# Performance work log

Measured on AMD Instinct MI355X. Metric: run time of the kernel, lower is better.

Reference implementation:

```python
import jax, jax.numpy as jnp
import numpy as np

N = 50000   # nodes
E = 100000  # directed edges
G = 2048    # graphs in batch
D = 32      # hidden dim
F_NODE = 11
F_EDGE = 4


def setup_inputs() -> dict:
    key = jax.random.key(0)
    ks = jax.random.split(key, 12)
    s = 0.1
    return {
        "x": jax.random.normal(ks[0], (N, F_NODE), dtype=jnp.float32),
        "edge_attr": jax.random.uniform(ks[1], (E, F_EDGE), dtype=jnp.float32),
        "lin0_w": jax.random.normal(ks[2], (D, F_NODE), dtype=jnp.float32) * s,
        "lin0_b": jnp.zeros((D,), jnp.float32),
        "nn_w": jax.random.normal(ks[3], (D * D, F_EDGE), dtype=jnp.float32) * s,
        "nn_b": jnp.zeros((D * D,), jnp.float32),
        "root_w": jax.random.normal(ks[4], (D, D), dtype=jnp.float32) * s,
        "conv_b": jnp.zeros((D,), jnp.float32),
        "gru_wi": jax.random.normal(ks[5], (3 * D, D), dtype=jnp.float32) * s,
        "gru_wh": jax.random.normal(ks[6], (3 * D, D), dtype=jnp.float32) * s,
        "gru_bi": jnp.zeros((3 * D,), jnp.float32),
        "gru_bh": jnp.zeros((3 * D,), jnp.float32),
        "lin1_w": jax.random.normal(ks[7], (2, D), dtype=jnp.float32) * s,
        "lin1_b": jnp.zeros((2,), jnp.float32),
        "edge_index": jax.random.randint(ks[8], (2, E), 0, N, dtype=jnp.int32),
        "batch": jnp.sort(jax.random.randint(ks[9], (N,), 0, G, dtype=jnp.int32)),
    }


def _gru_step(m, h, wi, wh, bi, bh):
    # single-step torch.nn.GRU cell math
    gi = m @ wi.T + bi            # [N, 3D]
    gh = h @ wh.T + bh            # [N, 3D]
    ir, iz, inn = jnp.split(gi, 3, axis=-1)
    hr, hz, hn = jnp.split(gh, 3, axis=-1)
    r = jax.nn.sigmoid(ir + hr)
    z = jax.nn.sigmoid(iz + hz)
    n = jnp.tanh(inn + r * hn)
    return (1.0 - z) * n + z * h


def reference(x, edge_attr, lin0_w, lin0_b, nn_w, nn_b, root_w, conv_b,
              gru_wi, gru_wh, gru_bi, gru_bh, lin1_w, lin1_b,
              edge_index, batch):
    src, dst = edge_index[0], edge_index[1]
    out = jax.nn.relu(x @ lin0_w.T + lin0_b)   # [N, D]
    h = out
    # per-edge 32x32 weight from edge MLP (edge_attr fixed -> hoisted out of loop)
    W_e = (edge_attr @ nn_w.T + nn_b).reshape(E, D, D)
    for _ in range(3):
        msg = jnp.einsum('ei,eio->eo', out[src], W_e)                  # [E, D]
        aggr = jax.ops.segment_sum(msg, dst, num_segments=N)           # add-aggregate
        m = jax.nn.relu(aggr + out @ root_w + conv_b)                  # NNConv root + bias
        h = _gru_step(m, h, gru_wi, gru_wh, gru_bi, gru_bh)
        out = h
    cnt = jax.ops.segment_sum(jnp.ones((N,), x.dtype), batch, num_segments=G)
    pooled = jax.ops.segment_sum(out, batch, num_segments=G) / jnp.maximum(cnt, 1.0)[:, None]
    logits = pooled @ lin1_w.T + lin1_b                                # [G, 2]
    return jax.nn.log_softmax(logits, axis=1)
```

## Files before the change

### kernel.cpp

```cpp
#include <hip/hip_runtime.h>
#include <hip/hip_bf16.h>

#define NN 50000
#define EE 100000
#define GG 2048
#define NB2 391

typedef float v2f __attribute__((ext_vector_type(2)));
__device__ __forceinline__ v2f fma2(v2f a, float b, v2f c) {
    return __builtin_elementwise_fma(a, (v2f){b, b}, c);
}

__device__ __forceinline__ float b2f(unsigned short u) {
    union { unsigned int i; float f; } x; x.i = (unsigned int)u << 16; return x.f;
}
__device__ __forceinline__ unsigned short f2b(float f) {
    union { float f; unsigned int i; } x; x.f = f;
    unsigned int b = x.i + (0x7FFFu + ((x.i >> 16) & 1u));
    return (unsigned short)(b >> 16);
}

__global__ __launch_bounds__(256) void k_setup(
    const float* __restrict__ x, const float* __restrict__ lw,
    const float* __restrict__ lb, const float* __restrict__ nnw,
    const float* __restrict__ nnb, const float* __restrict__ rootw,
    const float* __restrict__ wi, const float* __restrict__ wh,
    const int* __restrict__ ei, float* __restrict__ feat,
    float* __restrict__ Wre, float4* __restrict__ rw4,
    float4* __restrict__ wi4, int* __restrict__ cnt) {
    int blk = blockIdx.x;
    int t = threadIdx.x;
    if (blk < 6250) {
        int idx = blk * 256 + t;
        if (idx >= NN * 32) return;
        int n = idx >> 5, o = idx & 31;
        const float* xr = x + n * 11;
        const float* wr = lw + o * 11;
        float acc = lb[o];
#pragma unroll
        for (int i = 0; i < 11; ++i) acc += xr[i] * wr[i];
        feat[idx] = fmaxf(acc, 0.f);
    } else if (blk < 6278) {
        int idx = (blk - 6250) * 256 + t;
        if (idx < 5120) {
            int c = idx >> 5, i = idx & 31;
            float v;
            if (c < 128) v = nnw[((i << 5) + (c & 31)) * 4 + (c >> 5)];
            else         v = nnb[(i << 5) + (c - 128)];
            Wre[idx] = v;
        } else if (idx < 6144) {
            int j = idx - 5120;
            int k = j >> 5, o = j & 31;
            rw4[j] = make_float4(rootw[k * 32 + o], wh[o * 32 + k],
                                 wh[(32 + o) * 32 + k], wh[(64 + o) * 32 + k]);
        } else if (idx < 7168) {
            int j = idx - 6144;
            int k = j >> 5, o = j & 31;
            wi4[j] = make_float4(wi[o * 32 + k], wi[(32 + o) * 32 + k],
                                 wi[(64 + o) * 32 + k], 0.f);
        }
    } else {
        int e = (blk - 6278) * 256 + t;
        if (e >= EE) return;
        atomicAdd(&cnt[ei[EE + e]], 1);
        atomicAdd(&cnt[NN + ei[e]], 1);
    }
}

__global__ __launch_bounds__(256) void k_scan1(const int* __restrict__ cnt,
                                               int* __restrict__ tmp,
                                               int* __restrict__ bsum) {
    __shared__ int sd[256];
    int t = threadIdx.x;
    int i = blockIdx.x * 256 + t;
    int v = (i < 2 * NN) ? cnt[i] : 0;
    sd[t] = v;
    __syncthreads();
#pragma unroll
    for (int off = 1; off < 256; off <<= 1) {
        int x = (t >= off) ? sd[t - off] : 0;
        __syncthreads();
        sd[t] += x;
        __syncthreads();
    }
    if (i < 2 * NN) tmp[i] = sd[t];
    if (t == 255) bsum[blockIdx.x] = sd[255];
}

__global__ __launch_bounds__(512) void k_scan2(int* __restrict__ bsum) {
    __shared__ int sd[512];
    int t = threadIdx.x;
    int v = (t < NB2) ? bsum[t] : 0;
    sd[t] = v;
    __syncthreads();
#pragma unroll
    for (int off = 1; off < 512; off <<= 1) {
        int x = (t >= off) ? sd[t - off] : 0;
        __syncthreads();
        sd[t] += x;
        __syncthreads();
    }
    if (t < NB2) bsum[t] = sd[t];
}

__global__ void k_scan3(const int* __restrict__ cnt, const int* __restrict__ tmp,
                        const int* __restrict__ bsum, int* __restrict__ row_ptr,
                        int* __restrict__ cursor, int* __restrict__ out_ptr,
                        int* __restrict__ cursor2) {
    int i = blockIdx.x * blockDim.x + threadIdx.x;
    if (i >= 2 * NN) return;
    int base = (blockIdx.x > 0) ? bsum[blockIdx.x - 1] : 0;
    int excl = base + tmp[i] - cnt[i];
    if (i < NN) {
        row_ptr[i] = excl;
        cursor[i] = excl;
        if (i == 0) row_ptr[NN] = EE;
    } else {
        int j = i - NN;
        out_ptr[j] = excl - EE;
        cursor2[j] = excl - EE;
        if (j == 0) out_ptr[NN] = EE;
    }
}

__global__ __launch_bounds__(256) void k_scatter_y(
    const int* __restrict__ ei, const float* __restrict__ ea,
    int* __restrict__ cursor, int* __restrict__ cursor2,
    int* __restrict__ esrc, float4* __restrict__ eea,
    int* __restrict__ oslot, float4* __restrict__ oea,
    const float* __restrict__ feat, const float* __restrict__ Wre,
    unsigned short* __restrict__ yb) {
    int blk = blockIdx.x;
    if (blk < 391) {
        int e = blk * 256 + threadIdx.x;
        if (e >= EE) return;
        int s = ei[e], d = ei[EE + e];
        float4 a = make_float4(ea[e * 4 + 0], ea[e * 4 + 1], ea[e * 4 + 2], ea[e * 4 + 3]);
        int slot = atomicAdd(&cursor[d], 1);
        esrc[slot] = s;
        eea[slot] = a;
        int pos = atomicAdd(&cursor2[s], 1);
        oslot[pos] = slot;
        oea[pos] = a;
        return;
    }
    int by = blk - 391;
    int bx = by % 782, q = by / 782;
    int lane = threadIdx.x & 63;
    int wv = __builtin_amdgcn_readfirstlane(threadIdx.x >> 6);
    int n = bx * 64 + lane;
    if (n >= NN) return;
    int c0 = q * 40 + wv * 10;
    float fr[32];
    const float4* f4 = (const float4*)(feat + (long)n * 32);
#pragma unroll
    for (int qq = 0; qq < 8; ++qq) {
        float4 v = f4[qq];
        fr[4 * qq + 0] = v.x; fr[4 * qq + 1] = v.y;
        fr[4 * qq + 2] = v.z; fr[4 * qq + 3] = v.w;
    }
    float acc[10];
#pragma unroll
    for (int cc = 0; cc < 10; ++cc) {
        const float* w = Wre + (c0 + cc) * 32;
        float a = 0.f;
#pragma unroll
        for (int i = 0; i < 32; ++i) a += fr[i] * w[i];
        acc[cc] = a;
    }
    unsigned short* yr = yb + (long)n * 160 + c0;
#pragma unroll
    for (int qq = 0; qq < 5; ++qq) {
        unsigned int wlo = f2b(acc[2 * qq]);
        unsigned int whi = f2b(acc[2 * qq + 1]);
        ((unsigned int*)yr)[qq] = wlo | (whi << 16);
    }
}

__global__ __launch_bounds__(256) void k_conv_update(
    const unsigned short* __restrict__ msg_in, const int* __restrict__ row_ptr,
    const float4* __restrict__ rw4, const float* __restrict__ convb,
    const float4* __restrict__ wi4, const float* __restrict__ bi,
    const float* __restrict__ bh, const float4* __restrict__ nnw4,
    const float* __restrict__ nnb, const int* __restrict__ out_ptr,
    const int* __restrict__ oslot, const float4* __restrict__ oea,
    const unsigned short* __restrict__ yb, const int* __restrict__ esrc,
    const float4* __restrict__ eea,
    float* __restrict__ feat, unsigned short* __restrict__ msg_out,
    int gather_from_y, int write_msg) {
    __shared__ float fsT[32][36];
    __shared__ float msT[32][36];
    int t = threadIdx.x;
    int g = t >> 5, o = t & 31;
    int gc = g * 4;
    int nb = blockIdx.x * 32 + gc;
    float f[4], m[4];
    float cb = convb[o];
#pragma unroll
    for (int j = 0; j < 4; ++j) {
        int n = nb + j;
        bool v = (n < NN);
        f[j] = v ? feat[n * 32 + o] : 0.f;
        m[j] = cb;
        if (v) {
            int e0 = row_ptr[n], e1 = row_ptr[n + 1];
            if (gather_from_y) {
                for (int e = e0; e < e1; ++e) {
                    int s = esrc[e];
                    float4 a = eea[e];
                    const unsigned short* yr = yb + (long)s * 160;
                    float y0 = b2f(yr[o]);
                    float y1 = b2f(yr[32 + o]);
                    float y2 = b2f(yr[64 + o]);
                    float y3 = b2f(yr[96 + o]);
                    float y4 = b2f(yr[128 + o]);
                    m[j] += y4 + a.x * y0 + a.y * y1 + a.z * y2 + a.w * y3;
                }
            } else {
                for (int e = e0; e < e1; ++e)
                    m[j] += b2f(msg_in[(e << 5) + o]);
            }
        }
    }
    *(float4*)&fsT[o][gc] = make_float4(f[0], f[1], f[2], f[3]);
    __syncthreads();

    float bhr = bh[o], bhz = bh[32 + o], bhn = bh[64 + o];
    v2f m01 = {m[0], m[1]}, m23 = {m[2], m[3]};
    v2f ghr01 = {bhr, bhr}, ghr23 = {bhr, bhr};
    v2f ghz01 = {bhz, bhz}, ghz23 = {bhz, bhz};
    v2f ghn01 = {bhn, bhn}, ghn23 = {bhn, bhn};
#pragma unroll 4
    for (int i = 0; i < 32; ++i) {
        float4 w = rw4[i * 32 + o];
        float4 fv = *(const float4*)&fsT[i][gc];
        v2f f01 = {fv.x, fv.y}, f23 = {fv.z, fv.w};
        m01 = fma2(f01, w.x, m01);   m23 = fma2(f23, w.x, m23);
        ghr01 = fma2(f01, w.y, ghr01); ghr23 = fma2(f23, w.y, ghr23);
        ghz01 = fma2(f01, w.z, ghz01); ghz23 = fma2(f23, w.z, ghz23);
        ghn01 = fma2(f01, w.w, ghn01); ghn23 = fma2(f23, w.w, ghn23);
    }
    float mm0 = fmaxf(m01.x, 0.f), mm1 = fmaxf(m01.y, 0.f);
    float mm2 = fmaxf(m23.x, 0.f), mm3 = fmaxf(m23.y, 0.f);
    *(float4*)&msT[o][gc] = make_float4(mm0, mm1, mm2, mm3);
    __syncthreads();

    float bir = bi[o], biz = bi[32 + o], bin_ = bi[64 + o];
    v2f gir01 = {bir, bir}, gir23 = {bir, bir};
    v2f giz01 = {biz, biz}, giz23 = {biz, biz};
    v2f gin01 = {bin_, bin_}, gin23 = {bin_, bin_};
#pragma unroll 4
    for (int k = 0; k < 32; ++k) {
        float4 w = wi4[k * 32 + o];
        float4 mv = *(const float4*)&msT[k][gc];
        v2f p01 = {mv.x, mv.y}, p23 = {mv.z, mv.w};
        gir01 = fma2(p01, w.x, gir01); gir23 = fma2(p23, w.x, gir23);
        giz01 = fma2(p01, w.y, giz01); giz23 = fma2(p23, w.y, giz23);
        gin01 = fma2(p01, w.z, gin01); gin23 = fma2(p23, w.z, gin23);
    }
    float girA[4] = {gir01.x, gir01.y, gir23.x, gir23.y};
    float gizA[4] = {giz01.x, giz01.y, giz23.x, giz23.y};
    float ginA[4] = {gin01.x, gin01.y, gin23.x, gin23.y};
    float ghrA[4] = {ghr01.x, ghr01.y, ghr23.x, ghr23.y};
    float ghzA[4] = {ghz01.x, ghz01.y, ghz23.x, ghz23.y};
    float ghnA[4] = {ghn01.x, ghn01.y, ghn23.x, ghn23.y};
    float fn[4];
#pragma unroll
    for (int j = 0; j < 4; ++j) {
        int n = nb + j;
        float r = 1.f / (1.f + __expf(-(girA[j] + ghrA[j])));
        float z = 1.f / (1.f + __expf(-(gizA[j] + ghzA[j])));
        float nt = tanhf(ginA[j] + r * ghnA[j]);
        fn[j] = (1.f - z) * nt + z * f[j];
        if (n < NN) feat[n * 32 + o] = fn[j];
    }
    if (!write_msg) return;

    *(float4*)&fsT[o][gc] = make_float4(fn[0], fn[1], fn[2], fn[3]);
    v2f y0_01 = {0.f, 0.f}, y0_23 = {0.f, 0.f};
    v2f y1_01 = {0.f, 0.f}, y1_23 = {0.f, 0.f};
    v2f y2_01 = {0.f, 0.f}, y2_23 = {0.f, 0.f};
    v2f y3_01 = {0.f, 0.f}, y3_23 = {0.f, 0.f};
    v2f y4_01 = {0.f, 0.f}, y4_23 = {0.f, 0.f};
#pragma unroll 4
    for (int i = 0; i < 32; ++i) {
        float4 w = nnw4[i * 32 + o];
        float w1 = nnb[i * 32 + o];
        float4 fv = *(const float4*)&fsT[i][gc];
        v2f f01 = {fv.x, fv.y}, f23 = {fv.z, fv.w};
        y0_01 = fma2(f01, w.x, y0_01); y0_23 = fma2(f23, w.x, y0_23);
        y1_01 = fma2(f01, w.y, y1_01); y1_23 = fma2(f23, w.y, y1_23);
        y2_01 = fma2(f01, w.z, y2_01); y2_23 = fma2(f23, w.z, y2_23);
        y3_01 = fma2(f01, w.w, y3_01); y3_23 = fma2(f23, w.w, y3_23);
        y4_01 = fma2(f01, w1, y4_01);  y4_23 = fma2(f23, w1, y4_23);
    }
    float ya0[4] = {y0_01.x, y0_01.y, y0_23.x, y0_23.y};
    float ya1[4] = {y1_01.x, y1_01.y, y1_23.x, y1_23.y};
    float ya2[4] = {y2_01.x, y2_01.y, y2_23.x, y2_23.y};
    float ya3[4] = {y3_01.x, y3_01.y, y3_23.x, y3_23.y};
    float ya4[4] = {y4_01.x, y4_01.y, y4_23.x, y4_23.y};
#pragma unroll
    for (int j = 0; j < 4; ++j) {
        int n = nb + j;
        if (n < NN) {
            int p0 = out_ptr[n], p1 = out_ptr[n + 1];
            for (int p = p0; p < p1; ++p) {
                float4 a = oea[p];
                int slot = oslot[p];
                msg_out[(slot << 5) + o] =
                    f2b(ya4[j] + a.x * ya0[j] + a.y * ya1[j]
                               + a.z * ya2[j] + a.w * ya3[j]);
            }
        }
    }
}

__global__ __launch_bounds__(64) void k_pool_final(
    const float* __restrict__ feat, const int* __restrict__ batch,
    const float* __restrict__ w, const float* __restrict__ b,
    float* __restrict__ out) {
    int g = blockIdx.x;
    int t = threadIdx.x;
    int o = t & 31, h = t >> 5;
    int lo = 0, hi = NN;
    while (lo < hi) { int mid = (lo + hi) >> 1; if (batch[mid] < g) lo = mid + 1; else hi = mid; }
    int start = lo;
    hi = NN;
    while (lo < hi) { int mid = (lo + hi) >> 1; if (batch[mid] <= g) lo = mid + 1; else hi = mid; }
    int end = lo;
    float acc = 0.f;
    for (int n = start + h; n < end; n += 2) acc += feat[(long)n * 32 + o];
    acc += __shfl_xor(acc, 32, 64);
    float p = acc / fmaxf((float)(end - start), 1.f);
    float l0 = p * w[o], l1 = p * w[32 + o];
#pragma unroll
    for (int s = 16; s >= 1; s >>= 1) {
        l0 += __shfl_xor(l0, s, 64);
        l1 += __shfl_xor(l1, s, 64);
    }
    if (t == 0) {
        l0 += b[0]; l1 += b[1];
        float mx = fmaxf(l0, l1);
        float lse = mx + logf(__expf(l0 - mx) + __expf(l1 - mx));
        out[g * 2 + 0] = l0 - lse;
        out[g * 2 + 1] = l1 - lse;
    }
}

extern "C" void kernel_launch(void* const* d_in, const int* in_sizes, int n_in,
                              void* d_out, int out_size, void* d_ws, size_t ws_size,
                              hipStream_t stream) {
    const float* x        = (const float*)d_in[0];
    const float* edge_attr= (const float*)d_in[1];
    const float* lin0_w   = (const float*)d_in[2];
    const float* lin0_b   = (const float*)d_in[3];
    const float* nn_w     = (const float*)d_in[4];
    const float* nn_b     = (const float*)d_in[5];
    const float* root_w   = (const float*)d_in[6];
    const float* conv_b   = (const float*)d_in[7];
    const float* gru_wi   = (const float*)d_in[8];
    const float* gru_wh   = (const float*)d_in[9];
    const float* gru_bi   = (const float*)d_in[10];
    const float* gru_bh   = (const float*)d_in[11];
    const float* lin1_w   = (const float*)d_in[12];
    const float* lin1_b   = (const float*)d_in[13];
    const int*   edge_idx = (const int*)d_in[14];
    const int*   batch    = (const int*)d_in[15];
    float* out = (float*)d_out;

    float4* rw4   = (float4*)d_ws;
    float4* wi4   = rw4 + 1024;
    float4* eea   = wi4 + 1024;
    float4* oea   = eea + EE;
    float*  feat  = (float*)(oea + EE);
    float*  Wre   = feat + (long)NN * 32;
    int*    cnt   = (int*)(Wre + 5120);
    int*    tmp   = cnt + 2 * NN;
    int*    bsum  = tmp + 2 * NN;
    int*    row_ptr = bsum + 512;
    int*    cursor  = row_ptr + NN + 1;
    int*    out_ptr = cursor + NN;
    int*    cursor2 = out_ptr + NN + 1;
    int*    esrc  = cursor2 + NN;
    int*    oslot = esrc + EE;
    unsigned short* yb   = (unsigned short*)(oslot + EE);
    unsigned short* msgA = yb + (long)NN * 160;
    unsigned short* msgB = msgA + (long)EE * 32;
    const float4* nnw4 = (const float4*)nn_w;

    hipMemsetAsync(cnt, 0, 2 * NN * sizeof(int), stream);

    k_setup<<<6250 + 28 + 391, 256, 0, stream>>>(x, lin0_w, lin0_b, nn_w, nn_b,
                                                 root_w, gru_wi, gru_wh, edge_idx,
                                                 feat, Wre, rw4, wi4, cnt);

    k_scan1<<<NB2, 256, 0, stream>>>(cnt, tmp, bsum);
    k_scan2<<<1, 512, 0, stream>>>(bsum);
    k_scan3<<<NB2, 256, 0, stream>>>(cnt, tmp, bsum, row_ptr, cursor, out_ptr, cursor2);

    k_scatter_y<<<391 + 782 * 4, 256, 0, stream>>>(edge_idx, edge_attr, cursor, cursor2,
                                                   esrc, eea, oslot, oea, feat, Wre, yb);

    k_conv_update<<<(NN + 31) / 32, 256, 0, stream>>>(msgA, row_ptr, rw4, conv_b, wi4,
                                                      gru_bi, gru_bh, nnw4, nn_b,
                                                      out_ptr, oslot, oea,
                                                      yb, esrc, eea,
                                                      feat, msgB, 1, 1);
    k_conv_update<<<(NN + 31) / 32, 256, 0, stream>>>(msgB, row_ptr, rw4, conv_b, wi4,
                                                      gru_bi, gru_bh, nnw4, nn_b,
                                                      out_ptr, oslot, oea,
                                                      yb, esrc, eea,
                                                      feat, msgA, 0, 1);
    k_conv_update<<<(NN + 31) / 32, 256, 0, stream>>>(msgA, row_ptr, rw4, conv_b, wi4,
                                                      gru_bi, gru_bh, nnw4, nn_b,
                                                      out_ptr, oslot, oea,
                                                      yb, esrc, eea,
                                                      feat, msgB, 0, 0);

    k_pool_final<<<GG, 64, 0, stream>>>(feat, batch, lin1_w, lin1_b, out);
}
```

Measured before the change: 266.4 us.

## Template conv-update on nodes per group and store edge messages in fp32

The conv/GRU update kernel is now templated on nodes per thread group. Layers 2 and 3 use 8 nodes per group (64 per block) so each weight load is reused across more nodes, while layer 1 keeps 4. The per-edge message buffers switch from bf16 to fp32, which removes the pack and unpack work and the rounding but doubles message memory traffic. The larger tile also raises register use and halves the block count for those launches.

```diff
diff --git a/kernel.cpp b/kernel.cpp
--- a/kernel.cpp
+++ b/kernel.cpp
@@ -177,8 +177,9 @@
     }
 }
 
+template <int NPG>
 __global__ __launch_bounds__(256) void k_conv_update(
-    const unsigned short* __restrict__ msg_in, const int* __restrict__ row_ptr,
+    const float* __restrict__ msg_in, const int* __restrict__ row_ptr,
     const float4* __restrict__ rw4, const float* __restrict__ convb,
     const float4* __restrict__ wi4, const float* __restrict__ bi,
     const float* __restrict__ bh, const float4* __restrict__ nnw4,
@@ -186,18 +187,21 @@
     const int* __restrict__ oslot, const float4* __restrict__ oea,
     const unsigned short* __restrict__ yb, const int* __restrict__ esrc,
     const float4* __restrict__ eea,
-    float* __restrict__ feat, unsigned short* __restrict__ msg_out,
+    float* __restrict__ feat, float* __restrict__ msg_out,
     int gather_from_y, int write_msg) {
-    __shared__ float fsT[32][36];
-    __shared__ float msT[32][36];
+    constexpr int NH = NPG / 2;
+    constexpr int NQ = NPG / 4;
+    constexpr int ROW = 8 * NPG + 4;
+    __shared__ float fsT[32][ROW];
+    __shared__ float msT[32][ROW];
     int t = threadIdx.x;
     int g = t >> 5, o = t & 31;
-    int gc = g * 4;
-    int nb = blockIdx.x * 32 + gc;
-    float f[4], m[4];
+    int gc = g * NPG;
+    int nb = blockIdx.x * (8 * NPG) + gc;
+    float f[NPG], m[NPG];
     float cb = convb[o];
 #pragma unroll
-    for (int j = 0; j < 4; ++j) {
+    for (int j = 0; j < NPG; ++j) {
         int n = nb + j;
         bool v = (n < NN);
         f[j] = v ? feat[n * 32 + o] : 0.f;
@@ -218,89 +222,150 @@
                 }
             } else {
                 for (int e = e0; e < e1; ++e)
-                    m[j] += b2f(msg_in[(e << 5) + o]);
+                    m[j] += msg_in[(e << 5) + o];
             }
         }
     }
-    *(float4*)&fsT[o][gc] = make_float4(f[0], f[1], f[2], f[3]);
+#pragma unroll
+    for (int q = 0; q < NQ; ++q)
+        *(float4*)&fsT[o][gc + 4 * q] =
+            make_float4(f[4 * q], f[4 * q + 1], f[4 * q + 2], f[4 * q + 3]);
     __syncthreads();
 
     float bhr = bh[o], bhz = bh[32 + o], bhn = bh[64 + o];
-    v2f m01 = {m[0], m[1]}, m23 = {m[2], m[3]};
-    v2f ghr01 = {bhr, bhr}, ghr23 = {bhr, bhr};
-    v2f ghz01 = {bhz, bhz}, ghz23 = {bhz, bhz};
-    v2f ghn01 = {bhn, bhn}, ghn23 = {bhn, bhn};
-#pragma unroll 4
+    v2f m2[NH], ghr2[NH], ghz2[NH], ghn2[NH];
+#pragma unroll
+    for (int h = 0; h < NH; ++h) {
+        m2[h] = (v2f){m[2 * h], m[2 * h + 1]};
+        ghr2[h] = (v2f){bhr, bhr};
+        ghz2[h] = (v2f){bhz, bhz};
+        ghn2[h] = (v2f){bhn, bhn};
+    }
+#pragma unroll 2
     for (int i = 0; i < 32; ++i) {
         float4 w = rw4[i * 32 + o];
-        float4 fv = *(const float4*)&fsT[i][gc];
-        v2f f01 = {fv.x, fv.y}, f23 = {fv.z, fv.w};
-        m01 = fma2(f01, w.x, m01);   m23 = fma2(f23, w.x, m23);
-        ghr01 = fma2(f01, w.y, ghr01); ghr23 = fma2(f23, w.y, ghr23);
-        ghz01 = fma2(f01, w.z, ghz01); ghz23 = fma2(f23, w.z, ghz23);
-        ghn01 = fma2(f01, w.w, ghn01); ghn23 = fma2(f23, w.w, ghn23);
-    }
-    float mm0 = fmaxf(m01.x, 0.f), mm1 = fmaxf(m01.y, 0.f);
-    float mm2 = fmaxf(m23.x, 0.f), mm3 = fmaxf(m23.y, 0.f);
-    *(float4*)&msT[o][gc] = make_float4(mm0, mm1, mm2, mm3);
+        float4 fvq[NQ];
+#pragma unroll
+        for (int q = 0; q < NQ; ++q) fvq[q] = *(const float4*)&fsT[i][gc + 4 * q];
+        v2f f2[NH];
+#pragma unroll
+        for (int q = 0; q < NQ; ++q) {
+            f2[2 * q] = (v2f){fvq[q].x, fvq[q].y};
+            f2[2 * q + 1] = (v2f){fvq[q].z, fvq[q].w};
+        }
+#pragma unroll
+        for (int h = 0; h < NH; ++h) {
+            m2[h] = fma2(f2[h], w.x, m2[h]);
+            ghr2[h] = fma2(f2[h], w.y, ghr2[h]);
+            ghz2[h] = fma2(f2[h], w.z, ghz2[h]);
+            ghn2[h] = fma2(f2[h], w.w, ghn2[h]);
+        }
+    }
+    float mm[NPG];
+#pragma unroll
+    for (int h = 0; h < NH; ++h) {
+        mm[2 * h] = fmaxf(m2[h].x, 0.f);
+        mm[2 * h + 1] = fmaxf(m2[h].y, 0.f);
+    }
+#pragma unroll
+    for (int q = 0; q < NQ; ++q)
+        *(float4*)&msT[o][gc + 4 * q] =
+            make_float4(mm[4 * q], mm[4 * q + 1], mm[4 * q + 2], mm[4 * q + 3]);
     __syncthreads();
 
     float bir = bi[o], biz = bi[32 + o], bin_ = bi[64 + o];
-    v2f gir01 = {bir, bir}, gir23 = {bir, bir};
-    v2f giz01 = {biz, biz}, giz23 = {biz, biz};
-    v2f gin01 = {bin_, bin_}, gin23 = {bin_, bin_};
-#pragma unroll 4
+    v2f gir2[NH], giz2[NH], gin2[NH];
+#pragma unroll
+    for (int h = 0; h < NH; ++h) {
+        gir2[h] = (v2f){bir, bir};
+        giz2[h] = (v2f){biz, biz};
+        gin2[h] = (v2f){bin_, bin_};
+    }
+#pragma unroll 2
     for (int k = 0; k < 32; ++k) {
         float4 w = wi4[k * 32 + o];
-        float4 mv = *(const float4*)&msT[k][gc];
-        v2f p01 = {mv.x, mv.y}, p23 = {mv.z, mv.w};
-        gir01 = fma2(p01, w.x, gir01); gir23 = fma2(p23, w.x, gir23);
-        giz01 = fma2(p01, w.y, giz01); giz23 = fma2(p23, w.y, giz23);
-        gin01 = fma2(p01, w.z, gin01); gin23 = fma2(p23, w.z, gin23);
-    }
-    float girA[4] = {gir01.x, gir01.y, gir23.x, gir23.y};
-    float gizA[4] = {giz01.x, giz01.y, giz23.x, giz23.y};
-    float ginA[4] = {gin01.x, gin01.y, gin23.x, gin23.y};
-    float ghrA[4] = {ghr01.x, ghr01.y, ghr23.x, ghr23.y};
-    float ghzA[4] = {ghz01.x, ghz01.y, ghz23.x, ghz23.y};
-    float ghnA[4] = {ghn01.x, ghn01.y, ghn23.x, ghn23.y};
-    float fn[4];
-#pragma unroll
-    for (int j = 0; j < 4; ++j) {
-        int n = nb + j;
-        float r = 1.f / (1.f + __expf(-(girA[j] + ghrA[j])));
-        float z = 1.f / (1.f + __expf(-(gizA[j] + ghzA[j])));
-        float nt = tanhf(ginA[j] + r * ghnA[j]);
-        fn[j] = (1.f - z) * nt + z * f[j];
-        if (n < NN) feat[n * 32 + o] = fn[j];
+        float4 mvq[NQ];
+#pragma unroll
+        for (int q = 0; q < NQ; ++q) mvq[q] = *(const float4*)&msT[k][gc + 4 * q];
+        v2f p2[NH];
+#pragma unroll
+        for (int q = 0; q < NQ; ++q) {
+            p2[2 * q] = (v2f){mvq[q].x, mvq[q].y};
+            p2[2 * q + 1] = (v2f){mvq[q].z, mvq[q].w};
+        }
+#pragma unroll
+        for (int h = 0; h < NH; ++h) {
+            gir2[h] = fma2(p2[h], w.x, gir2[h]);
+            giz2[h] = fma2(p2[h], w.y, giz2[h]);
+            gin2[h] = fma2(p2[h], w.z, gin2[h]);
+        }
+    }
+    float fn[NPG];
+#pragma unroll
+    for (int h = 0; h < NH; ++h) {
+        float girA[2] = {gir2[h].x, gir2[h].y};
+        float gizA[2] = {giz2[h].x, giz2[h].y};
+        float ginA[2] = {gin2[h].x, gin2[h].y};
+        float ghrA[2] = {ghr2[h].x, ghr2[h].y};
+        float ghzA[2] = {ghz2[h].x, ghz2[h].y};
+        float ghnA[2] = {ghn2[h].x, ghn2[h].y};
+#pragma unroll
+        for (int c = 0; c < 2; ++c) {
+            int j = 2 * h + c;
+            float r = 1.f / (1.f + __expf(-(girA[c] + ghrA[c])));
+            float z = 1.f / (1.f + __expf(-(gizA[c] + ghzA[c])));
+            float nt = tanhf(ginA[c] + r * ghnA[c]);
+            fn[j] = (1.f - z) * nt + z * f[j];
+            int n = nb + j;
+            if (n < NN) feat[n * 32 + o] = fn[j];
+        }
     }
     if (!write_msg) return;
 
-    *(float4*)&fsT[o][gc] = make_float4(fn[0], fn[1], fn[2], fn[3]);
-    v2f y0_01 = {0.f, 0.f}, y0_23 = {0.f, 0.f};
-    v2f y1_01 = {0.f, 0.f}, y1_23 = {0.f, 0.f};
-    v2f y2_01 = {0.f, 0.f}, y2_23 = {0.f, 0.f};
-    v2f y3_01 = {0.f, 0.f}, y3_23 = {0.f, 0.f};
-    v2f y4_01 = {0.f, 0.f}, y4_23 = {0.f, 0.f};
-#pragma unroll 4
+#pragma unroll
+    for (int q = 0; q < NQ; ++q)
+        *(float4*)&fsT[o][gc + 4 * q] =
+            make_float4(fn[4 * q], fn[4 * q + 1], fn[4 * q + 2], fn[4 * q + 3]);
+    v2f y0a[NH], y1a[NH], y2a[NH], y3a[NH], y4a[NH];
+#pragma unroll
+    for (int h = 0; h < NH; ++h) {
+        y0a[h] = (v2f){0.f, 0.f}; y1a[h] = (v2f){0.f, 0.f};
+        y2a[h] = (v2f){0.f, 0.f}; y3a[h] = (v2f){0.f, 0.f};
+        y4a[h] = (v2f){0.f, 0.f};
+    }
+#pragma unroll 2
     for (int i = 0; i < 32; ++i) {
         float4 w = nnw4[i * 32 + o];
         float w1 = nnb[i * 32 + o];
-        float4 fv = *(const float4*)&fsT[i][gc];
-        v2f f01 = {fv.x, fv.y}, f23 = {fv.z, fv.w};
-        y0_01 = fma2(f01, w.x, y0_01); y0_23 = fma2(f23, w.x, y0_23);
-        y1_01 = fma2(f01, w.y, y1_01); y1_23 = fma2(f23, w.y, y1_23);
-        y2_01 = fma2(f01, w.z, y2_01); y2_23 = fma2(f23, w.z, y2_23);
-        y3_01 = fma2(f01, w.w, y3_01); y3_23 = fma2(f23, w.w, y3_23);
-        y4_01 = fma2(f01, w1, y4_01);  y4_23 = fma2(f23, w1, y4_23);
-    }
-    float ya0[4] = {y0_01.x, y0_01.y, y0_23.x, y0_23.y};
-    float ya1[4] = {y1_01.x, y1_01.y, y1_23.x, y1_23.y};
-    float ya2[4] = {y2_01.x, y2_01.y, y2_23.x, y2_23.y};
-    float ya3[4] = {y3_01.x, y3_01.y, y3_23.x, y3_23.y};
-    float ya4[4] = {y4_01.x, y4_01.y, y4_23.x, y4_23.y};
-#pragma unroll
-    for (int j = 0; j < 4; ++j) {
+        float4 fvq[NQ];
+#pragma unroll
+        for (int q = 0; q < NQ; ++q) fvq[q] = *(const float4*)&fsT[i][gc + 4 * q];
+        v2f f2[NH];
+#pragma unroll
+        for (int q = 0; q < NQ; ++q) {
+            f2[2 * q] = (v2f){fvq[q].x, fvq[q].y};
+            f2[2 * q + 1] = (v2f){fvq[q].z, fvq[q].w};
+        }
+#pragma unroll
+        for (int h = 0; h < NH; ++h) {
+            y0a[h] = fma2(f2[h], w.x, y0a[h]);
+            y1a[h] = fma2(f2[h], w.y, y1a[h]);
+            y2a[h] = fma2(f2[h], w.z, y2a[h]);
+            y3a[h] = fma2(f2[h], w.w, y3a[h]);
+            y4a[h] = fma2(f2[h], w1, y4a[h]);
+        }
+    }
+    float ya0[NPG], ya1[NPG], ya2[NPG], ya3[NPG], ya4[NPG];
+#pragma unroll
+    for (int h = 0; h < NH; ++h) {
+        ya0[2 * h] = y0a[h].x; ya0[2 * h + 1] = y0a[h].y;
+        ya1[2 * h] = y1a[h].x; ya1[2 * h + 1] = y1a[h].y;
+        ya2[2 * h] = y2a[h].x; ya2[2 * h + 1] = y2a[h].y;
+        ya3[2 * h] = y3a[h].x; ya3[2 * h + 1] = y3a[h].y;
+        ya4[2 * h] = y4a[h].x; ya4[2 * h + 1] = y4a[h].y;
+    }
+#pragma unroll
+    for (int j = 0; j < NPG; ++j) {
         int n = nb + j;
         if (n < NN) {
             int p0 = out_ptr[n], p1 = out_ptr[n + 1];
@@ -308,8 +373,8 @@
                 float4 a = oea[p];
                 int slot = oslot[p];
                 msg_out[(slot << 5) + o] =
-                    f2b(ya4[j] + a.x * ya0[j] + a.y * ya1[j]
-                               + a.z * ya2[j] + a.w * ya3[j]);
+                    ya4[j] + a.x * ya0[j] + a.y * ya1[j]
+                           + a.z * ya2[j] + a.w * ya3[j];
             }
         }
     }
@@ -383,9 +448,10 @@
     int*    cursor2 = out_ptr + NN + 1;
     int*    esrc  = cursor2 + NN;
     int*    oslot = esrc + EE;
-    unsigned short* yb   = (unsigned short*)(oslot + EE);
-    unsigned short* msgA = yb + (long)NN * 160;
-    unsigned short* msgB = msgA + (long)EE * 32;
+    unsigned short* yb = (unsigned short*)(oslot + EE);
+    size_t moff = ((size_t)((char*)(yb + (long)NN * 160) - (char*)d_ws) + 15) & ~(size_t)15;
+    float*  msgA = (float*)((char*)d_ws + moff);
+    float*  msgB = msgA + (long)EE * 32;
     const float4* nnw4 = (const float4*)nn_w;
 
     hipMemsetAsync(cnt, 0, 2 * NN * sizeof(int), stream);
@@ -401,21 +467,15 @@
     k_scatter_y<<<391 + 782 * 4, 256, 0, stream>>>(edge_idx, edge_attr, cursor, cursor2,
                                                    esrc, eea, oslot, oea, feat, Wre, yb);
 
-    k_conv_update<<<(NN + 31) / 32, 256, 0, stream>>>(msgA, row_ptr, rw4, conv_b, wi4,
-                                                      gru_bi, gru_bh, nnw4, nn_b,
-                                                      out_ptr, oslot, oea,
-                                                      yb, esrc, eea,
-                                                      feat, msgB, 1, 1);
-    k_conv_update<<<(NN + 31) / 32, 256, 0, stream>>>(msgB, row_ptr, rw4, conv_b, wi4,
-                                                      gru_bi, gru_bh, nnw4, nn_b,
-                                                      out_ptr, oslot, oea,
-                                                      yb, esrc, eea,
-                                                      feat, msgA, 0, 1);
-    k_conv_update<<<(NN + 31) / 32, 256, 0, stream>>>(msgA, row_ptr, rw4, conv_b, wi4,
-                                                      gru_bi, gru_bh, nnw4, nn_b,
-                                                      out_ptr, oslot, oea,
-                                                      yb, esrc, eea,
-                                                      feat, msgB, 0, 0);
+    k_conv_update<4><<<(NN + 31) / 32, 256, 0, stream>>>(
+        msgA, row_ptr, rw4, conv_b, wi4, gru_bi, gru_bh, nnw4, nn_b,
+        out_ptr, oslot, oea, yb, esrc, eea, feat, msgB, 1, 1);
+    k_conv_update<8><<<(NN + 63) / 64, 256, 0, stream>>>(
+        msgB, row_ptr, rw4, conv_b, wi4, gru_bi, gru_bh, nnw4, nn_b,
+        out_ptr, oslot, oea, yb, esrc, eea, feat, msgA, 0, 1);
+    k_conv_update<8><<<(NN + 63) / 64, 256, 0, stream>>>(
+        msgA, row_ptr, rw4, conv_b, wi4, gru_bi, gru_bh, nnw4, nn_b,
+        out_ptr, oslot, oea, yb, esrc, eea, feat, msgB, 0, 0);
 
     k_pool_final<<<GG, 64, 0, stream>>>(feat, batch, lin1_w, lin1_b, out);
 }
```

Result: no change. 269.7 us (+1.3%).
